# Kernel tuning notes

Hardware: AMD Instinct MI355X
Metric: run time of the kernel (lower is better)

The kernel has to match this reference:

```python
import jax, jax.numpy as jnp
import numpy as np

K_ORDER, NUM_HEADS, BETA = 4, 2, 0.5
D_IN, D_OUT = 64, 64


def _batch_and_pos(n_nodes, N):
    # batch[i] = graph id of node i; pos[i] = index of node i within its graph
    batch = jnp.repeat(jnp.arange(n_nodes.shape[0], dtype=jnp.int32), n_nodes, total_repeat_length=N)
    ptr = jnp.concatenate([jnp.zeros(1, jnp.int32), jnp.cumsum(n_nodes).astype(jnp.int32)])
    pos = jnp.arange(N, dtype=jnp.int32) - ptr[batch]
    return batch, pos


def _to_pad(feat, batch, pos, Bsz, max_node):
    out_shape = (Bsz, max_node) + feat.shape[1:]
    return jnp.zeros(out_shape, feat.dtype).at[batch, pos].set(feat)


def fast_attn_conv(qs, ks, vs, n_nodes, batch, pos, max_node):
    # qs/ks/vs: [N,H,D]; linear attention with per-graph kv outer-product sums
    Bsz = n_nodes.shape[0]
    q_pad = _to_pad(qs, batch, pos, Bsz, max_node)  # [B,M,H,D]
    k_pad = _to_pad(ks, batch, pos, Bsz, max_node)
    v_pad = _to_pad(vs, batch, pos, Bsz, max_node)
    kv = jnp.einsum('bnhd,bnhe->bdhe', k_pad, v_pad)  # [B,D,H,D]
    v_sum = jax.ops.segment_sum(vs, batch, num_segments=Bsz)  # [B,H,D]
    k_sum = jax.ops.segment_sum(ks, batch, num_segments=Bsz)  # [B,H,D]
    numerator = jnp.einsum('bnhd,bdhe->bnhe', q_pad, kv)[batch, pos] + v_sum[batch]
    denom = jnp.einsum('bnhd,bhd->bnh', q_pad, k_sum)[batch, pos]
    denom = denom + n_nodes.astype(qs.dtype)[batch][:, None]
    return numerator / denom[..., None]


def gcn_conv(x, edge_index, e_feat):
    # x: [N,H,D], e_feat: [E,D]
    N = x.shape[0]
    row, col = edge_index[0], edge_index[1]
    deg = jax.ops.segment_sum(jnp.ones(row.shape[0], x.dtype), row, num_segments=N)
    dis = jnp.where(deg > 0, deg ** -0.5, jnp.zeros_like(deg))
    w = dis[row] * dis[col]  # [E]
    msg_edge = jax.ops.segment_sum(w[:, None] * e_feat, row, num_segments=N)  # [N,D]
    new_feat = jax.ops.segment_sum(x[col] * w[:, None, None], row, num_segments=N)  # [N,H,D]
    return new_feat + msg_edge[:, None, :]


def setup_inputs():
    key = jax.random.key(0)
    ks = jax.random.split(key, 10)
    B = 64
    n_nodes_np = np.tile(np.array([1000, 2000], np.int32), B // 2)  # sums to 96000
    N = int(n_nodes_np.sum())
    E = 768000
    x = jax.random.normal(ks[0], (N, D_IN), jnp.float32)
    edge_index = jax.random.randint(ks[1], (2, E), 0, N, jnp.int32)
    edge_attr = jax.random.randint(ks[2], (E, 3), 0, 8, jnp.int32)
    s = 0.02
    Wq_w = jax.random.normal(ks[3], (D_IN * NUM_HEADS, D_IN), jnp.float32) * s
    Wq_b = jnp.zeros((D_IN * NUM_HEADS,), jnp.float32)
    Wk_w = jax.random.normal(ks[4], (D_IN * NUM_HEADS, D_IN), jnp.float32) * s
    Wk_b = jnp.zeros((D_IN * NUM_HEADS,), jnp.float32)
    Wo_w = jax.random.normal(ks[5], (D_OUT, D_IN * NUM_HEADS), jnp.float32) * s
    Wo_b = jnp.zeros((D_OUT,), jnp.float32)
    bond_emb = jax.random.normal(ks[6], (3, 8, D_OUT), jnp.float32) * s
    return {"x": x, "Wq_w": Wq_w, "Wq_b": Wq_b, "Wk_w": Wk_w, "Wk_b": Wk_b,
            "Wo_w": Wo_w, "Wo_b": Wo_b, "bond_emb": bond_emb,
            "edge_index": edge_index, "edge_attr": edge_attr,
            "n_nodes": jnp.asarray(n_nodes_np)}


def reference(x, Wq_w, Wq_b, Wk_w, Wk_b, Wo_w, Wo_b, bond_emb, edge_index, edge_attr, n_nodes):
    N = x.shape[0]
    max_node = 2000  # static max over n_nodes
    batch, pos = _batch_and_pos(n_nodes, N)
    query = (x @ Wq_w.T + Wq_b).reshape(N, NUM_HEADS, D_IN)
    key_t = (x @ Wk_w.T + Wk_b).reshape(N, NUM_HEADS, D_IN)
    qs = query / jnp.linalg.norm(query, axis=2, keepdims=True)
    kk = key_t / jnp.linalg.norm(key_t, axis=2, keepdims=True)
    # BondEncoder: sum of per-feature embeddings
    e_feat = bond_emb[0][edge_attr[:, 0]] + bond_emb[1][edge_attr[:, 1]] + bond_emb[2][edge_attr[:, 2]]
    h = jnp.broadcast_to(x[:, None, :], (N, NUM_HEADS, D_IN))
    acc = h
    cur = h
    for _ in range(K_ORDER):
        gcn_i = gcn_conv(cur, edge_index, e_feat)
        attn_i = fast_attn_conv(qs, kk, cur, n_nodes, batch, pos, max_node)
        cur = BETA * gcn_i + (1.0 - BETA) * attn_i
        acc = acc + cur
    out = acc.reshape(N, NUM_HEADS * D_IN)
    return (out @ Wo_w.T + Wo_b) / NUM_HEADS
```

## Files before the change

kernel.cpp:

```cpp
#include <hip/hip_runtime.h>
#include <hip/hip_bf16.h>


typedef __attribute__((ext_vector_type(8))) short bf16x8;
typedef __attribute__((ext_vector_type(4))) float f32x4v;

#define CHUNK 100

__device__ __forceinline__ float asf(unsigned int u) { union { unsigned int i; float f; } v; v.i = u; return v.f; }
__device__ __forceinline__ float b2f_u(unsigned short u) { return asf((unsigned int)u << 16); }
__device__ __forceinline__ unsigned short f2b_u(float f) {
    __hip_bfloat16 h = __float2bfloat16(f);
    union { __hip_bfloat16 h; unsigned short u; } v; v.h = h; return v.u;
}
__device__ __forceinline__ unsigned int pack2(float a, float b) {
    return (unsigned int)f2b_u(a) | ((unsigned int)f2b_u(b) << 16);
}
__device__ __forceinline__ float wave_reduce_sum(float v) {
    #pragma unroll
    for (int off = 32; off > 0; off >>= 1) v += __shfl_xor(v, off, 64);
    return v;
}

__global__ void k_ptr(const int* __restrict__ nn, int* __restrict__ ptr,
                      int* __restrict__ cptr, int* __restrict__ tptr, int B) {
    if (threadIdx.x == 0 && blockIdx.x == 0) {
        int s = 0, c = 0, t = 0; ptr[0] = 0; cptr[0] = 0; tptr[0] = 0;
        for (int i = 0; i < B; ++i) {
            s += nn[i]; ptr[i + 1] = s;
            c += (nn[i] + CHUNK - 1) / CHUNK; cptr[i + 1] = c;
            t += (nn[i] + 15) / 16; tptr[i + 1] = t;
        }
    }
}

__global__ void k_batch(const int* __restrict__ ptr, int* __restrict__ batch) {
    int b = blockIdx.x;
    int s = ptr[b], e = ptr[b + 1];
    for (int i = s + threadIdx.x; i < e; i += blockDim.x) batch[i] = b;
}

__global__ void k_wcvt(const float* __restrict__ Wq_w, const float* __restrict__ Wk_w,
                       const float* __restrict__ Wo_w, unsigned short* __restrict__ Wb) {
    int i = blockIdx.x * 256 + threadIdx.x;
    if (i < 24576) {
        float v = (i < 8192) ? Wq_w[i] : ((i < 16384) ? Wk_w[i - 8192] : Wo_w[i - 16384]);
        Wb[i] = f2b_u(v);
    }
}

__global__ __launch_bounds__(256) void k_qkm(
    const float* __restrict__ x, const unsigned short* __restrict__ Wb,
    const float* __restrict__ Wq_b, const float* __restrict__ Wk_b,
    unsigned short* __restrict__ q, unsigned short* __restrict__ kq,
    unsigned short* __restrict__ curA, int N)
{
    int w = threadIdx.x >> 6, l = threadIdx.x & 63;
    int six = l & 15, quad = l >> 4;
    int base = (blockIdx.x * 4 + w) * 16;
    if (base >= N) return;
    int n = base + six;
    int nc = min(n, N - 1);

    const float* xr = x + (size_t)nc * 64;
    float xv0[8], xv1[8];
    #pragma unroll
    for (int j = 0; j < 8; ++j) { xv0[j] = xr[quad * 8 + j]; xv1[j] = xr[32 + quad * 8 + j]; }
    union { bf16x8 v; unsigned int u[4]; } b0, b1;
    #pragma unroll
    for (int i = 0; i < 4; ++i) {
        b0.u[i] = pack2(xv0[2 * i], xv0[2 * i + 1]);
        b1.u[i] = pack2(xv1[2 * i], xv1[2 * i + 1]);
    }
    if (n < N) {
        unsigned short* cr = curA + (size_t)n * 128;
        *(uint4*)(cr + quad * 8)       = make_uint4(b0.u[0], b0.u[1], b0.u[2], b0.u[3]);
        *(uint4*)(cr + 32 + quad * 8)  = make_uint4(b1.u[0], b1.u[1], b1.u[2], b1.u[3]);
        *(uint4*)(cr + 64 + quad * 8)  = make_uint4(b0.u[0], b0.u[1], b0.u[2], b0.u[3]);
        *(uint4*)(cr + 96 + quad * 8)  = make_uint4(b1.u[0], b1.u[1], b1.u[2], b1.u[3]);
    }

    #pragma unroll
    for (int g = 0; g < 4; ++g) {
        f32x4v c[4];
        #pragma unroll
        for (int tt = 0; tt < 4; ++tt) {
            int t = g * 4 + tt;
            const unsigned short* wr = Wb + (size_t)(t * 16 + six) * 64;
            bf16x8 a0 = *(const bf16x8*)(wr + quad * 8);
            bf16x8 a1 = *(const bf16x8*)(wr + 32 + quad * 8);
            f32x4v cc = {0.f, 0.f, 0.f, 0.f};
            cc = __builtin_amdgcn_mfma_f32_16x16x32_bf16(a0, b0.v, cc, 0, 0, 0);
            cc = __builtin_amdgcn_mfma_f32_16x16x32_bf16(a1, b1.v, cc, 0, 0, 0);
            c[tt] = cc;
        }
        const float* bias = (g < 2) ? Wq_b : Wk_b;
        int cb = (g & 1) * 64 + quad * 4;
        float ss = 0.f;
        #pragma unroll
        for (int tt = 0; tt < 4; ++tt)
            #pragma unroll
            for (int r = 0; r < 4; ++r) {
                float v = c[tt][r] + bias[cb + tt * 16 + r];
                c[tt][r] = v;
                ss += v * v;
            }
        ss += __shfl_xor(ss, 16, 64);
        ss += __shfl_xor(ss, 32, 64);
        float sc = rsqrtf(ss);
        if (n < N) {
            unsigned short* dst = ((g < 2) ? q : kq) + (size_t)n * 128;
            #pragma unroll
            for (int tt = 0; tt < 4; ++tt) {
                unsigned int u0 = pack2(c[tt][0] * sc, c[tt][1] * sc);
                unsigned int u1 = pack2(c[tt][2] * sc, c[tt][3] * sc);
                *(uint2*)(dst + cb + tt * 16) = make_uint2(u0, u1);
            }
        }
    }
}

__global__ void k_deg(const int* __restrict__ row, int* __restrict__ deg,
                      int* __restrict__ slot, int E) {
    int e = blockIdx.x * 256 + threadIdx.x;
    if (e < E) slot[e] = atomicAdd(&deg[row[e]], 1);
}

__global__ void k_dis(const int* __restrict__ deg, float* __restrict__ dis, int N) {
    int n = blockIdx.x * 256 + threadIdx.x;
    if (n < N) { int d = deg[n]; dis[n] = d > 0 ? rsqrtf((float)d) : 0.f; }
}

__global__ void k_scan1(const int* __restrict__ deg, int* __restrict__ rowstart,
                        int* __restrict__ bsum, int N) {
    __shared__ int sh[256];
    int t = threadIdx.x, n = blockIdx.x * 256 + t;
    int v = (n < N) ? deg[n] : 0;
    sh[t] = v; __syncthreads();
    #pragma unroll
    for (int off = 1; off < 256; off <<= 1) {
        int add = (t >= off) ? sh[t - off] : 0;
        __syncthreads();
        sh[t] += add;
        __syncthreads();
    }
    if (n < N) rowstart[n] = sh[t] - v;
    if (t == 255) bsum[blockIdx.x] = sh[255];
}

__global__ void k_scan2(int* __restrict__ bsum, int nb) {
    __shared__ int sh[512];
    __shared__ int carry;
    int t = threadIdx.x;
    if (t == 0) carry = 0;
    __syncthreads();
    for (int base = 0; base < nb; base += 512) {
        int idx = base + t;
        int v = (idx < nb) ? bsum[idx] : 0;
        sh[t] = v; __syncthreads();
        for (int off = 1; off < 512; off <<= 1) {
            int add = (t >= off) ? sh[t - off] : 0;
            __syncthreads();
            sh[t] += add;
            __syncthreads();
        }
        if (idx < nb) bsum[idx] = sh[t] - v + carry;
        __syncthreads();
        if (t == 0) carry += sh[511];
        __syncthreads();
    }
}

__global__ void k_scan3(int* __restrict__ rowstart, const int* __restrict__ bsum, int N, int E) {
    int n = blockIdx.x * 256 + threadIdx.x;
    if (n < N) rowstart[n] += bsum[blockIdx.x];
    if (n == 0) rowstart[N] = E;
}

__global__ void k_fill(const int* __restrict__ eidx, const float* __restrict__ dis,
                       const int* __restrict__ rowstart, const int* __restrict__ slot,
                       int4* __restrict__ csr_pack, const int* __restrict__ eattr, int E) {
    int e = blockIdx.x * 256 + threadIdx.x;
    if (e >= E) return;
    int r = eidx[e], c = eidx[E + e];
    float wv = dis[r] * dis[c];
    int a0 = eattr[e * 3 + 0], a1 = eattr[e * 3 + 1], a2 = eattr[e * 3 + 2];
    int idx = rowstart[r] + slot[e];
    int4 v;
    v.x = c;
    v.y = __float_as_int(wv);
    v.z = a0 | (a1 << 8) | (a2 << 16);
    v.w = 0;
    csr_pack[idx] = v;
}

__global__ __launch_bounds__(256) void k_msg(
    const int* __restrict__ rowstart, const int4* __restrict__ csr_pack,
    const float* __restrict__ bond, unsigned short* __restrict__ msgb, int N) {
    __shared__ float bl[1536];
    int t = threadIdx.x, w = t >> 6, l = t & 63;
    for (int i = t; i < 1536; i += 256) bl[i] = bond[i];
    __syncthreads();
    for (int n = blockIdx.x * 4 + w; n < N; n += gridDim.x * 4) {
        int s0 = rowstart[n], s1 = rowstart[n + 1];
        float m = 0.f;
        #pragma unroll 4
        for (int i = s0; i < s1; ++i) {
            int4 pk = csr_pack[i];
            float wv = __int_as_float(pk.y);
            int att = pk.z;
            m += wv * (bl[(att & 255) * 64 + l] + bl[(8 + ((att >> 8) & 255)) * 64 + l]
                     + bl[(16 + (att >> 16)) * 64 + l]);
        }
        msgb[(size_t)n * 64 + l] = f2b_u(m);
    }
}

__global__ __launch_bounds__(256) void k_ksump(
    const unsigned short* __restrict__ kq, const int* __restrict__ ptr,
    const int* __restrict__ cptr, float* __restrict__ partKS, int B)
{
    int cid = blockIdx.x;
    if (cid >= cptr[B]) return;
    int lo = 0, hi = B - 1;
    while (lo < hi) { int mid = (lo + hi + 1) >> 1; if (cptr[mid] <= cid) lo = mid; else hi = mid - 1; }
    int b = lo;
    int start = ptr[b] + (cid - cptr[b]) * CHUNK;
    int end = min(start + CHUNK, ptr[b + 1]);
    int t = threadIdx.x, r = t >> 7, col = t & 127;
    float a = 0.f;
    for (int n = start + r; n < end; n += 2)
        a += b2f_u(kq[(size_t)n * 128 + col]);
    __shared__ float sh[256];
    sh[t] = a;
    __syncthreads();
    if (t < 128) partKS[(size_t)cid * 128 + t] = sh[t] + sh[t + 128];
}

__global__ __launch_bounds__(128) void k_ksr(
    const float* __restrict__ partKS, const int* __restrict__ cptr,
    float* __restrict__ ksum, int B)
{
    int b = blockIdx.x, t = threadIdx.x;
    float s = 0.f;
    int c0 = cptr[b], c1 = cptr[b + 1];
    for (int c = c0; c < c1; ++c) s += partKS[(size_t)c * 128 + t];
    ksum[b * 128 + t] = s;
}

__global__ __launch_bounds__(256) void k_denom(
    const unsigned short* __restrict__ q, const float* __restrict__ ksum,
    const int* __restrict__ batch, const int* __restrict__ nn,
    float* __restrict__ denom, int N)
{
    int w = threadIdx.x >> 6, l = threadIdx.x & 63;
    int n = blockIdx.x * 4 + w;
    if (n >= N) return;
    int b = batch[n];
    float d0 = b2f_u(q[(size_t)n * 128 + l]) * ksum[b * 128 + l];
    float d1 = b2f_u(q[(size_t)n * 128 + 64 + l]) * ksum[b * 128 + 64 + l];
    d0 = wave_reduce_sum(d0);
    d1 = wave_reduce_sum(d1);
    if (l == 0) {
        float nf = (float)nn[b];
        denom[n * 2 + 0] = d0 + nf;
        denom[n * 2 + 1] = d1 + nf;
    }
}

__global__ __launch_bounds__(256) void k_kvp(
    const unsigned short* __restrict__ kq, const unsigned short* __restrict__ cur,
    const int* __restrict__ ptr, const int* __restrict__ cptr,
    unsigned short* __restrict__ partKV, float* __restrict__ partVS, int B)
{
    int cid = blockIdx.x;
    if (cid >= cptr[B]) return;
    int lo = 0, hi = B - 1;
    while (lo < hi) { int mid = (lo + hi + 1) >> 1; if (cptr[mid] <= cid) lo = mid; else hi = mid - 1; }
    int b = lo;
    int start = ptr[b] + (cid - cptr[b]) * CHUNK;
    int end = min(start + CHUNK, ptr[b + 1]);

    int w = threadIdx.x >> 6, l = threadIdx.x & 63;
    int h = w >> 1, dhalf = w & 1;
    int d0 = dhalf * 32 + (l & 7) * 4;
    int e0 = (l >> 3) * 8;
    float a[4][8], va[8];
    #pragma unroll
    for (int i = 0; i < 4; ++i)
        #pragma unroll
        for (int j = 0; j < 8; ++j) a[i][j] = 0.f;
    #pragma unroll
    for (int j = 0; j < 8; ++j) va[j] = 0.f;

    const unsigned short* kp = kq + (size_t)start * 128 + h * 64 + d0;
    const unsigned short* vp = cur + (size_t)start * 128 + h * 64 + e0;
    #pragma unroll 4
    for (int n = start; n < end; ++n) {
        uint2 ku = *(const uint2*)kp;
        uint4 vu = *(const uint4*)vp;
        kp += 128; vp += 128;
        float k0 = asf(ku.x << 16), k1 = asf(ku.x & 0xffff0000u);
        float k2 = asf(ku.y << 16), k3 = asf(ku.y & 0xffff0000u);
        float v[8];
        v[0] = asf(vu.x << 16); v[1] = asf(vu.x & 0xffff0000u);
        v[2] = asf(vu.y << 16); v[3] = asf(vu.y & 0xffff0000u);
        v[4] = asf(vu.z << 16); v[5] = asf(vu.z & 0xffff0000u);
        v[6] = asf(vu.w << 16); v[7] = asf(vu.w & 0xffff0000u);
        #pragma unroll
        for (int j = 0; j < 8; ++j) {
            a[0][j] += k0 * v[j]; a[1][j] += k1 * v[j];
            a[2][j] += k2 * v[j]; a[3][j] += k3 * v[j];
            va[j] += v[j];
        }
    }
    unsigned short* dst = partKV + (size_t)cid * 8192 + h * 4096;
    #pragma unroll
    for (int j = 0; j < 8; ++j) {
        uint2 s2 = make_uint2(pack2(a[0][j], a[1][j]), pack2(a[2][j], a[3][j]));
        *(uint2*)(dst + (e0 + j) * 64 + d0) = s2;
    }
    if (dhalf == 0 && (l & 7) == 0) {
        float* vdst = partVS + (size_t)cid * 128 + h * 64 + e0;
        #pragma unroll
        for (int j = 0; j < 8; ++j) vdst[j] = va[j];
    }
}

__global__ __launch_bounds__(256) void k_red(
    const unsigned short* __restrict__ partKV, const float* __restrict__ partVS,
    const int* __restrict__ cptr, unsigned short* __restrict__ kvT_b,
    float* __restrict__ vsum, int B)
{
    int bid = blockIdx.x;
    int gh = bid >> 1, half = bid & 1;
    int g = gh >> 1, h = gh & 1;
    int c0 = cptr[g], c1 = cptr[g + 1];
    int t = threadIdx.x;
    int off = half * 2048 + t * 8;
    float s[8];
    #pragma unroll
    for (int i = 0; i < 8; ++i) s[i] = 0.f;
    for (int c = c0; c < c1; ++c) {
        uint4 u = *(const uint4*)(partKV + (size_t)c * 8192 + h * 4096 + off);
        s[0] += asf(u.x << 16); s[1] += asf(u.x & 0xffff0000u);
        s[2] += asf(u.y << 16); s[3] += asf(u.y & 0xffff0000u);
        s[4] += asf(u.z << 16); s[5] += asf(u.z & 0xffff0000u);
        s[6] += asf(u.w << 16); s[7] += asf(u.w & 0xffff0000u);
    }
    unsigned int u[4];
    #pragma unroll
    for (int i = 0; i < 4; ++i) u[i] = pack2(s[2 * i], s[2 * i + 1]);
    *(uint4*)(kvT_b + (size_t)gh * 4096 + off) = make_uint4(u[0], u[1], u[2], u[3]);
    if (half == 0 && t < 64) {
        float vs = 0.f;
        for (int c = c0; c < c1; ++c) vs += partVS[(size_t)c * 128 + h * 64 + t];
        vsum[g * 128 + h * 64 + t] = vs;
    }
}

__global__ __launch_bounds__(256) void k_attn(
    const unsigned short* __restrict__ q, const unsigned short* __restrict__ kvT,
    const float* __restrict__ vsum, const float* __restrict__ denom,
    const int* __restrict__ ptr, const int* __restrict__ tptr,
    const unsigned short* __restrict__ msgb,
    unsigned short* __restrict__ curB, int B)
{
    int w = threadIdx.x >> 6, l = threadIdx.x & 63;
    int tid = blockIdx.x * 4 + w;
    if (tid >= tptr[B]) return;
    int lo = 0, hi = B - 1;
    while (lo < hi) { int mid = (lo + hi + 1) >> 1; if (tptr[mid] <= tid) lo = mid; else hi = mid - 1; }
    int b0 = lo;
    int start = ptr[b0] + (tid - tptr[b0]) * 16;
    int end = min(start + 16, ptr[b0 + 1]);
    int quad = l >> 4, six = l & 15;
    int n = start + six;
    int nc = min(n, end - 1);
    bool live = n < end;
    const unsigned short* mrow = msgb + (size_t)nc * 64;
    uint2 me[4];
    #pragma unroll
    for (int et = 0; et < 4; ++et) me[et] = *(const uint2*)(mrow + et * 16 + quad * 4);
    #pragma unroll
    for (int h = 0; h < 2; ++h) {
        const unsigned short* qrow = q + (size_t)nc * 128 + h * 64;
        bf16x8 qb0 = *(const bf16x8*)(qrow + quad * 8);
        bf16x8 qb1 = *(const bf16x8*)(qrow + 32 + quad * 8);
        const unsigned short* Bb = kvT + (size_t)(b0 * 2 + h) * 4096;
        float dn = denom[nc * 2 + h];
        const float* vsb = vsum + (b0 * 2 + h) * 64;
        #pragma unroll
        for (int et = 0; et < 4; ++et) {
            const unsigned short* arow = Bb + (size_t)(et * 16 + six) * 64;
            bf16x8 a0 = *(const bf16x8*)(arow + quad * 8);
            bf16x8 a1 = *(const bf16x8*)(arow + 32 + quad * 8);
            f32x4v c = {0.f, 0.f, 0.f, 0.f};
            c = __builtin_amdgcn_mfma_f32_16x16x32_bf16(a0, qb0, c, 0, 0, 0);
            c = __builtin_amdgcn_mfma_f32_16x16x32_bf16(a1, qb1, c, 0, 0, 0);
            float4 vs = *(const float4*)(vsb + et * 16 + quad * 4);
            float m0 = asf(me[et].x << 16), m1 = asf(me[et].x & 0xffff0000u);
            float m2 = asf(me[et].y << 16), m3 = asf(me[et].y & 0xffff0000u);
            float v0 = 0.5f * (c[0] + vs.x) / dn + 0.5f * m0;
            float v1 = 0.5f * (c[1] + vs.y) / dn + 0.5f * m1;
            float v2 = 0.5f * (c[2] + vs.z) / dn + 0.5f * m2;
            float v3 = 0.5f * (c[3] + vs.w) / dn + 0.5f * m3;
            if (live) {
                uint2 st = make_uint2(pack2(v0, v1), pack2(v2, v3));
                *(uint2*)(curB + (size_t)n * 128 + h * 64 + et * 16 + quad * 4) = st;
            }
        }
    }
}

__global__ __launch_bounds__(256) void k_gcn(
    const unsigned short* __restrict__ curA,
    const int* __restrict__ rowstart, const int4* __restrict__ csr_pack,
    unsigned short* __restrict__ curB, unsigned short* __restrict__ acc, int N, int first)
{
    int orig = blockIdx.x, nwg = gridDim.x;
    int q8 = nwg >> 3, r8 = nwg & 7;
    int xcd = orig & 7, jj = orig >> 3;
    int swz = (xcd < r8 ? xcd * (q8 + 1) : r8 * (q8 + 1) + (xcd - r8) * q8) + jj;

    int w = threadIdx.x >> 6, l = threadIdx.x & 63;
    int qq = l >> 4, ql = l & 15;
    int nA = swz * 8 + w * 2;
    if (nA >= N) return;
    bool hasB = (nA + 1) < N;
    int s0  = rowstart[nA];
    int sA1 = rowstart[nA + 1];
    int s1  = hasB ? rowstart[nA + 2] : sA1;

    int e0 = 8 * ql + 2 * qq;
    size_t oA = (size_t)nA * 128 + e0;
    size_t oB = (size_t)(nA + 1) * 128 + e0;
    const unsigned short* accsrc = first ? curA : acc;
    unsigned int ubA = *(const unsigned int*)(curB + oA);
    unsigned int uaA = *(const unsigned int*)(accsrc + oA);
    unsigned int ubB = 0, uaB = 0;
    if (hasB) {
        ubB = *(const unsigned int*)(curB + oB);
        uaB = *(const unsigned int*)(accsrc + oB);
    }

    float gT[8], gA[8];
    #pragma unroll
    for (int j = 0; j < 8; ++j) { gT[j] = 0.f; gA[j] = 0.f; }
    const int2* cw2 = (const int2*)csr_pack;
    #pragma unroll 4
    for (int i = s0 + qq; i < s1; i += 4) {
        int2 cw = cw2[2 * i];
        float wv = __int_as_float(cw.y);
        float wvA = (i < sA1) ? wv : 0.f;
        uint4 u = *(const uint4*)(curA + (size_t)cw.x * 128 + 8 * ql);
        float v0 = asf(u.x << 16), v1 = asf(u.x & 0xffff0000u);
        float v2 = asf(u.y << 16), v3 = asf(u.y & 0xffff0000u);
        float v4 = asf(u.z << 16), v5 = asf(u.z & 0xffff0000u);
        float v6 = asf(u.w << 16), v7 = asf(u.w & 0xffff0000u);
        gT[0] += wv * v0;  gA[0] += wvA * v0;
        gT[1] += wv * v1;  gA[1] += wvA * v1;
        gT[2] += wv * v2;  gA[2] += wvA * v2;
        gT[3] += wv * v3;  gA[3] += wvA * v3;
        gT[4] += wv * v4;  gA[4] += wvA * v4;
        gT[5] += wv * v5;  gA[5] += wvA * v5;
        gT[6] += wv * v6;  gA[6] += wvA * v6;
        gT[7] += wv * v7;  gA[7] += wvA * v7;
    }
    #pragma unroll
    for (int j = 0; j < 8; ++j) {
        gT[j] += __shfl_xor(gT[j], 16, 64);
        gT[j] += __shfl_xor(gT[j], 32, 64);
        gA[j] += __shfl_xor(gA[j], 16, 64);
        gA[j] += __shfl_xor(gA[j], 32, 64);
    }
    float a0 = (qq == 0) ? gA[0] : (qq == 1) ? gA[2] : (qq == 2) ? gA[4] : gA[6];
    float a1 = (qq == 0) ? gA[1] : (qq == 1) ? gA[3] : (qq == 2) ? gA[5] : gA[7];
    float t0 = (qq == 0) ? gT[0] : (qq == 1) ? gT[2] : (qq == 2) ? gT[4] : gT[6];
    float t1 = (qq == 0) ? gT[1] : (qq == 1) ? gT[3] : (qq == 2) ? gT[5] : gT[7];
    float b0 = t0 - a0, b1 = t1 - a1;
    float vA0 = 0.5f * a0 + asf(ubA << 16);
    float vA1 = 0.5f * a1 + asf(ubA & 0xffff0000u);
    *(unsigned int*)(curB + oA) = pack2(vA0, vA1);
    *(unsigned int*)(acc + oA) = pack2(asf(uaA << 16) + vA0, asf(uaA & 0xffff0000u) + vA1);
    if (hasB) {
        float vB0 = 0.5f * b0 + asf(ubB << 16);
        float vB1 = 0.5f * b1 + asf(ubB & 0xffff0000u);
        *(unsigned int*)(curB + oB) = pack2(vB0, vB1);
        *(unsigned int*)(acc + oB) = pack2(asf(uaB << 16) + vB0, asf(uaB & 0xffff0000u) + vB1);
    }
}

__global__ __launch_bounds__(256) void k_outm(
    const unsigned short* __restrict__ acc, const unsigned short* __restrict__ Wob,
    const float* __restrict__ Wo_b, float* __restrict__ out, int N)
{
    int w = threadIdx.x >> 6, l = threadIdx.x & 63;
    int six = l & 15, quad = l >> 4;
    int base = (blockIdx.x * 4 + w) * 16;
    if (base >= N) return;
    int n = base + six;
    int nc = min(n, N - 1);
    const unsigned short* ar = acc + (size_t)nc * 128;
    bf16x8 b0 = *(const bf16x8*)(ar + quad * 8);
    bf16x8 b1 = *(const bf16x8*)(ar + 32 + quad * 8);
    bf16x8 b2 = *(const bf16x8*)(ar + 64 + quad * 8);
    bf16x8 b3 = *(const bf16x8*)(ar + 96 + quad * 8);
    #pragma unroll
    for (int t = 0; t < 4; ++t) {
        const unsigned short* wr = Wob + (size_t)(t * 16 + six) * 128;
        bf16x8 a0 = *(const bf16x8*)(wr + quad * 8);
        bf16x8 a1 = *(const bf16x8*)(wr + 32 + quad * 8);
        bf16x8 a2 = *(const bf16x8*)(wr + 64 + quad * 8);
        bf16x8 a3 = *(const bf16x8*)(wr + 96 + quad * 8);
        f32x4v c = {0.f, 0.f, 0.f, 0.f};
        c = __builtin_amdgcn_mfma_f32_16x16x32_bf16(a0, b0, c, 0, 0, 0);
        c = __builtin_amdgcn_mfma_f32_16x16x32_bf16(a1, b1, c, 0, 0, 0);
        c = __builtin_amdgcn_mfma_f32_16x16x32_bf16(a2, b2, c, 0, 0, 0);
        c = __builtin_amdgcn_mfma_f32_16x16x32_bf16(a3, b3, c, 0, 0, 0);
        if (n < N) {
            float4 bias = *(const float4*)(Wo_b + t * 16 + quad * 4);
            float4 o4;
            o4.x = (c[0] + bias.x) * 0.5f;
            o4.y = (c[1] + bias.y) * 0.5f;
            o4.z = (c[2] + bias.z) * 0.5f;
            o4.w = (c[3] + bias.w) * 0.5f;
            *(float4*)(out + (size_t)n * 64 + t * 16 + quad * 4) = o4;
        }
    }
}

extern "C" void kernel_launch(void* const* d_in, const int* in_sizes, int n_in,
                              void* d_out, int out_size, void* d_ws, size_t ws_size,
                              hipStream_t stream) {
    const float* x    = (const float*)d_in[0];
    const float* Wq_w = (const float*)d_in[1];
    const float* Wq_b = (const float*)d_in[2];
    const float* Wk_w = (const float*)d_in[3];
    const float* Wk_b = (const float*)d_in[4];
    const float* Wo_w = (const float*)d_in[5];
    const float* Wo_b = (const float*)d_in[6];
    const float* bond = (const float*)d_in[7];
    const int*   eidx = (const int*)d_in[8];
    const int*   eattr= (const int*)d_in[9];
    const int*   nn   = (const int*)d_in[10];
    float* out = (float*)d_out;
    int N = in_sizes[0] / 64;
    int E = in_sizes[9] / 3;
    int B = in_sizes[10];

    char* p = (char*)d_ws;
    auto alloc = [&](size_t bytes) { char* r = p; p += (bytes + 255) & ~(size_t)255; return r; };
    unsigned short* q    = (unsigned short*)alloc((size_t)N * 128 * 2);
    unsigned short* kq   = (unsigned short*)alloc((size_t)N * 128 * 2);
    unsigned short* curA = (unsigned short*)alloc((size_t)N * 128 * 2);
    unsigned short* curB = (unsigned short*)alloc((size_t)N * 128 * 2);
    unsigned short* acc  = (unsigned short*)alloc((size_t)N * 128 * 2);
    int maxchunks = (N + CHUNK - 1) / CHUNK + B;
    int maxtiles  = (N + 15) / 16 + B;
    unsigned short* partKV = (unsigned short*)alloc((size_t)maxchunks * 8192 * 2);
    float* partVS = (float*)alloc((size_t)maxchunks * 128 * 4);
    float* partKS = (float*)alloc((size_t)maxchunks * 128 * 4);
    unsigned short* kvT_b = (unsigned short*)alloc((size_t)B * 2 * 64 * 64 * 2);
    float* vsum  = (float*)alloc((size_t)B * 128 * 4);
    float* ksum  = (float*)alloc((size_t)B * 128 * 4);
    float* denom = (float*)alloc((size_t)N * 2 * 4);
    float* dis   = (float*)alloc((size_t)N * 4);
    int* deg     = (int*)alloc((size_t)N * 4);
    int* rowstart= (int*)alloc((size_t)(N + 1) * 4);
    int* slot    = (int*)alloc((size_t)E * 4);
    int4* csr_pack = (int4*)alloc((size_t)E * 16);
    int* batch   = (int*)alloc((size_t)N * 4);
    int* ptr     = (int*)alloc((size_t)(B + 1) * 4);
    int* cptr    = (int*)alloc((size_t)(B + 1) * 4);
    int* tptr    = (int*)alloc((size_t)(B + 1) * 4);
    unsigned short* Wb = (unsigned short*)alloc(24576 * 2);
    int nb = (N + 255) / 256;
    int* bsum    = (int*)alloc((size_t)nb * 4);
    unsigned short* msgb = (unsigned short*)out;

    hipMemsetAsync(deg, 0, (size_t)N * 4, stream);

    k_ptr  <<<1, 64, 0, stream>>>(nn, ptr, cptr, tptr, B);
    k_batch<<<B, 256, 0, stream>>>(ptr, batch);
    k_wcvt <<<96, 256, 0, stream>>>(Wq_w, Wk_w, Wo_w, Wb);
    k_qkm  <<<(N + 63) / 64, 256, 0, stream>>>(x, Wb, Wq_b, Wk_b, q, kq, curA, N);
    k_deg  <<<(E + 255) / 256, 256, 0, stream>>>(eidx, deg, slot, E);
    k_dis  <<<(N + 255) / 256, 256, 0, stream>>>(deg, dis, N);
    k_scan1<<<nb, 256, 0, stream>>>(deg, rowstart, bsum, N);
    k_scan2<<<1, 512, 0, stream>>>(bsum, nb);
    k_scan3<<<nb, 256, 0, stream>>>(rowstart, bsum, N, E);
    k_fill <<<(E + 255) / 256, 256, 0, stream>>>(eidx, dis, rowstart, slot, csr_pack, eattr, E);
    k_msg  <<<2048, 256, 0, stream>>>(rowstart, csr_pack, bond, msgb, N);
    k_ksump<<<maxchunks, 256, 0, stream>>>(kq, ptr, cptr, partKS, B);
    k_ksr  <<<B, 128, 0, stream>>>(partKS, cptr, ksum, B);
    k_denom<<<(N + 3) / 4, 256, 0, stream>>>(q, ksum, batch, nn, denom, N);

    int gcnblk = (N + 7) / 8;
    for (int it = 0; it < 4; ++it) {
        k_kvp <<<maxchunks, 256, 0, stream>>>(kq, curA, ptr, cptr, partKV, partVS, B);
        k_red <<<B * 4, 256, 0, stream>>>(partKV, partVS, cptr, kvT_b, vsum, B);
        k_attn<<<(maxtiles + 3) / 4, 256, 0, stream>>>(q, kvT_b, vsum, denom, ptr, tptr, msgb, curB, B);
        k_gcn <<<gcnblk, 256, 0, stream>>>(curA, rowstart, csr_pack, curB, acc, N, it == 0 ? 1 : 0);
        unsigned short* tmp = curA; curA = curB; curB = tmp;
    }
    k_outm<<<(N + 63) / 64, 256, 0, stream>>>(acc, Wb + 16384, Wo_b, out, N);
}
```

Before: 788.0 us.

## Split GCN gather per node half-wave, fuse dis into scan, enlarge chunk

The GCN gather kernel now gives each half-wave one node, with two lane-groups splitting that node's edges. This replaces the old scheme where all four lane-groups swept both nodes' edges and kept two sets of accumulators, so redundant FMAs and shuffles go away and stores become 8-byte. The separate degree-normalization kernel is folded into the first scan kernel, saving one launch. CHUNK is doubled, which changes the partitioning of the attention partial-sum kernels. Load balance may get worse when the two nodes in a wave have very different degrees, and each node's gather now has less memory-level parallelism.

```diff
diff --git a/kernel.cpp b/kernel.cpp
--- a/kernel.cpp
+++ b/kernel.cpp
@@ -5,7 +5,7 @@
 typedef __attribute__((ext_vector_type(8))) short bf16x8;
 typedef __attribute__((ext_vector_type(4))) float f32x4v;
 
-#define CHUNK 100
+#define CHUNK 200
 
 __device__ __forceinline__ float asf(unsigned int u) { union { unsigned int i; float f; } v; v.i = u; return v.f; }
 __device__ __forceinline__ float b2f_u(unsigned short u) { return asf((unsigned int)u << 16); }
@@ -126,16 +126,12 @@
     if (e < E) slot[e] = atomicAdd(&deg[row[e]], 1);
 }
 
-__global__ void k_dis(const int* __restrict__ deg, float* __restrict__ dis, int N) {
-    int n = blockIdx.x * 256 + threadIdx.x;
-    if (n < N) { int d = deg[n]; dis[n] = d > 0 ? rsqrtf((float)d) : 0.f; }
-}
-
 __global__ void k_scan1(const int* __restrict__ deg, int* __restrict__ rowstart,
-                        int* __restrict__ bsum, int N) {
+                        int* __restrict__ bsum, float* __restrict__ dis, int N) {
     __shared__ int sh[256];
     int t = threadIdx.x, n = blockIdx.x * 256 + t;
     int v = (n < N) ? deg[n] : 0;
+    if (n < N) dis[n] = v > 0 ? rsqrtf((float)v) : 0.f;
     sh[t] = v; __syncthreads();
     #pragma unroll
     for (int off = 1; off < 256; off <<= 1) {
@@ -425,69 +421,57 @@
 
     int w = threadIdx.x >> 6, l = threadIdx.x & 63;
     int qq = l >> 4, ql = l & 15;
+    int half = qq >> 1;
+    int par  = qq & 1;
     int nA = swz * 8 + w * 2;
     if (nA >= N) return;
     bool hasB = (nA + 1) < N;
+    int myN = nA + half;
+    bool live = myN < N;
     int s0  = rowstart[nA];
     int sA1 = rowstart[nA + 1];
     int s1  = hasB ? rowstart[nA + 2] : sA1;
-
-    int e0 = 8 * ql + 2 * qq;
-    size_t oA = (size_t)nA * 128 + e0;
-    size_t oB = (size_t)(nA + 1) * 128 + e0;
+    int base = half ? sA1 : s0;
+    int lim  = half ? s1  : sA1;
+
+    int e0 = 8 * ql + par * 4;
+    size_t o = (size_t)myN * 128 + e0;
     const unsigned short* accsrc = first ? curA : acc;
-    unsigned int ubA = *(const unsigned int*)(curB + oA);
-    unsigned int uaA = *(const unsigned int*)(accsrc + oA);
-    unsigned int ubB = 0, uaB = 0;
-    if (hasB) {
-        ubB = *(const unsigned int*)(curB + oB);
-        uaB = *(const unsigned int*)(accsrc + oB);
-    }
-
-    float gT[8], gA[8];
-    #pragma unroll
-    for (int j = 0; j < 8; ++j) { gT[j] = 0.f; gA[j] = 0.f; }
+    uint2 ub = make_uint2(0, 0), ua = make_uint2(0, 0);
+    if (live) {
+        ub = *(const uint2*)(curB + o);
+        ua = *(const uint2*)(accsrc + o);
+    }
+
+    float g[8];
+    #pragma unroll
+    for (int j = 0; j < 8; ++j) g[j] = 0.f;
     const int2* cw2 = (const int2*)csr_pack;
-    #pragma unroll 4
-    for (int i = s0 + qq; i < s1; i += 4) {
+    #pragma unroll 2
+    for (int i = base + par; i < lim; i += 2) {
         int2 cw = cw2[2 * i];
         float wv = __int_as_float(cw.y);
-        float wvA = (i < sA1) ? wv : 0.f;
         uint4 u = *(const uint4*)(curA + (size_t)cw.x * 128 + 8 * ql);
-        float v0 = asf(u.x << 16), v1 = asf(u.x & 0xffff0000u);
-        float v2 = asf(u.y << 16), v3 = asf(u.y & 0xffff0000u);
-        float v4 = asf(u.z << 16), v5 = asf(u.z & 0xffff0000u);
-        float v6 = asf(u.w << 16), v7 = asf(u.w & 0xffff0000u);
-        gT[0] += wv * v0;  gA[0] += wvA * v0;
-        gT[1] += wv * v1;  gA[1] += wvA * v1;
-        gT[2] += wv * v2;  gA[2] += wvA * v2;
-        gT[3] += wv * v3;  gA[3] += wvA * v3;
-        gT[4] += wv * v4;  gA[4] += wvA * v4;
-        gT[5] += wv * v5;  gA[5] += wvA * v5;
-        gT[6] += wv * v6;  gA[6] += wvA * v6;
-        gT[7] += wv * v7;  gA[7] += wvA * v7;
-    }
-    #pragma unroll
-    for (int j = 0; j < 8; ++j) {
-        gT[j] += __shfl_xor(gT[j], 16, 64);
-        gT[j] += __shfl_xor(gT[j], 32, 64);
-        gA[j] += __shfl_xor(gA[j], 16, 64);
-        gA[j] += __shfl_xor(gA[j], 32, 64);
-    }
-    float a0 = (qq == 0) ? gA[0] : (qq == 1) ? gA[2] : (qq == 2) ? gA[4] : gA[6];
-    float a1 = (qq == 0) ? gA[1] : (qq == 1) ? gA[3] : (qq == 2) ? gA[5] : gA[7];
-    float t0 = (qq == 0) ? gT[0] : (qq == 1) ? gT[2] : (qq == 2) ? gT[4] : gT[6];
-    float t1 = (qq == 0) ? gT[1] : (qq == 1) ? gT[3] : (qq == 2) ? gT[5] : gT[7];
-    float b0 = t0 - a0, b1 = t1 - a1;
-    float vA0 = 0.5f * a0 + asf(ubA << 16);
-    float vA1 = 0.5f * a1 + asf(ubA & 0xffff0000u);
-    *(unsigned int*)(curB + oA) = pack2(vA0, vA1);
-    *(unsigned int*)(acc + oA) = pack2(asf(uaA << 16) + vA0, asf(uaA & 0xffff0000u) + vA1);
-    if (hasB) {
-        float vB0 = 0.5f * b0 + asf(ubB << 16);
-        float vB1 = 0.5f * b1 + asf(ubB & 0xffff0000u);
-        *(unsigned int*)(curB + oB) = pack2(vB0, vB1);
-        *(unsigned int*)(acc + oB) = pack2(asf(uaB << 16) + vB0, asf(uaB & 0xffff0000u) + vB1);
+        g[0] += wv * asf(u.x << 16); g[1] += wv * asf(u.x & 0xffff0000u);
+        g[2] += wv * asf(u.y << 16); g[3] += wv * asf(u.y & 0xffff0000u);
+        g[4] += wv * asf(u.z << 16); g[5] += wv * asf(u.z & 0xffff0000u);
+        g[6] += wv * asf(u.w << 16); g[7] += wv * asf(u.w & 0xffff0000u);
+    }
+    #pragma unroll
+    for (int j = 0; j < 8; ++j) g[j] += __shfl_xor(g[j], 16, 64);
+    float s0v = par ? g[4] : g[0];
+    float s1v = par ? g[5] : g[1];
+    float s2v = par ? g[6] : g[2];
+    float s3v = par ? g[7] : g[3];
+    if (live) {
+        float v0 = 0.5f * s0v + asf(ub.x << 16);
+        float v1 = 0.5f * s1v + asf(ub.x & 0xffff0000u);
+        float v2 = 0.5f * s2v + asf(ub.y << 16);
+        float v3 = 0.5f * s3v + asf(ub.y & 0xffff0000u);
+        *(uint2*)(curB + o) = make_uint2(pack2(v0, v1), pack2(v2, v3));
+        float a0 = asf(ua.x << 16) + v0, a1 = asf(ua.x & 0xffff0000u) + v1;
+        float a2 = asf(ua.y << 16) + v2, a3 = asf(ua.y & 0xffff0000u) + v3;
+        *(uint2*)(acc + o) = make_uint2(pack2(a0, a1), pack2(a2, a3));
     }
 }
 
@@ -586,8 +570,7 @@
     k_wcvt <<<96, 256, 0, stream>>>(Wq_w, Wk_w, Wo_w, Wb);
     k_qkm  <<<(N + 63) / 64, 256, 0, stream>>>(x, Wb, Wq_b, Wk_b, q, kq, curA, N);
     k_deg  <<<(E + 255) / 256, 256, 0, stream>>>(eidx, deg, slot, E);
-    k_dis  <<<(N + 255) / 256, 256, 0, stream>>>(deg, dis, N);
-    k_scan1<<<nb, 256, 0, stream>>>(deg, rowstart, bsum, N);
+    k_scan1<<<nb, 256, 0, stream>>>(deg, rowstart, bsum, dis, N);
     k_scan2<<<1, 512, 0, stream>>>(bsum, nb);
     k_scan3<<<nb, 256, 0, stream>>>(rowstart, bsum, N, E);
     k_fill <<<(E + 255) / 256, 256, 0, stream>>>(eidx, dis, rowstart, slot, csr_pack, eattr, E);
```

After: 792.6 us. About the same (+0.6%).
